# Performance work log

Hardware: AMD Instinct MI355X
Metric: run time of the kernel (lower is better)

Reference implementation:

```python
import jax, jax.numpy as jnp
import numpy as np

HIDDEN = 3584
NUM_HEADS = 28
NUM_KV_HEADS = 4
HEAD_DIM = 128
ROPE_THETA = 1000000.0
B, S = 2, 2048


def setup_inputs() -> dict:
    key = jax.random.key(0)
    k1, k2, k3, k4 = jax.random.split(key, 4)
    q_size = NUM_HEADS * HEAD_DIM
    kv_size = NUM_KV_HEADS * HEAD_DIM
    return {
        "positions": jnp.arange(B * S, dtype=jnp.int32).reshape(B, S),
        "hidden_states": jax.random.normal(k1, (B, S, HIDDEN), dtype=jnp.float32),
        "w_qkv": jax.random.normal(k2, (HIDDEN, q_size + 2 * kv_size), dtype=jnp.float32) * (HIDDEN ** -0.5),
        "b_qkv": jax.random.normal(k3, (q_size + 2 * kv_size,), dtype=jnp.float32) * 0.02,
        "w_o": jax.random.normal(k4, (q_size, HIDDEN), dtype=jnp.float32) * (q_size ** -0.5),
    }


def _rope_cos_sin(positions):
    # NeoX-style rotary embedding, rotary_dim == head_dim
    half = HEAD_DIM // 2
    inv_freq = 1.0 / (ROPE_THETA ** (jnp.arange(0, half, dtype=jnp.float32) * 2.0 / HEAD_DIM))
    angles = positions.astype(jnp.float32)[..., None] * inv_freq  # [B, S, half]
    return jnp.cos(angles), jnp.sin(angles)


def _apply_rope(x, cos, sin):
    # x: [B, S, H, D]; cos/sin: [B, S, half] -> broadcast over heads
    x1, x2 = jnp.split(x, 2, axis=-1)
    c = cos[:, :, None, :]
    s = sin[:, :, None, :]
    return jnp.concatenate([x1 * c - x2 * s, x2 * c + x1 * s], axis=-1)


def reference(positions, hidden_states, w_qkv, b_qkv, w_o):
    q_size = NUM_HEADS * HEAD_DIM
    kv_size = NUM_KV_HEADS * HEAD_DIM
    scaling = HEAD_DIM ** -0.5
    groups = NUM_HEADS // NUM_KV_HEADS

    qkv = hidden_states @ w_qkv + b_qkv  # [B, S, q+2kv]
    q, k, v = jnp.split(qkv, [q_size, q_size + kv_size], axis=-1)
    q = q.reshape(B, S, NUM_HEADS, HEAD_DIM)
    k = k.reshape(B, S, NUM_KV_HEADS, HEAD_DIM)
    v = v.reshape(B, S, NUM_KV_HEADS, HEAD_DIM)

    cos, sin = _rope_cos_sin(positions)
    q = _apply_rope(q, cos, sin)
    k = _apply_rope(k, cos, sin)

    # GQA: group query heads over kv heads. q: [B, S, Hkv, G, D]
    qg = q.reshape(B, S, NUM_KV_HEADS, groups, HEAD_DIM)
    scores = jnp.einsum("bqhgd,bkhd->bhgqk", qg, k) * scaling  # [B, Hkv, G, S, S]
    causal = jnp.tril(jnp.ones((S, S), dtype=bool))
    scores = jnp.where(causal, scores, jnp.finfo(scores.dtype).min)
    probs = jax.nn.softmax(scores, axis=-1)
    o = jnp.einsum("bhgqk,bkhd->bqhgd", probs, v)  # [B, S, Hkv, G, D]
    o = o.reshape(B, S, NUM_HEADS * HEAD_DIM)
    return o @ w_o  # [B, S, HIDDEN]
```

## Files before the change

### kernel.cpp

```cpp
#include <hip/hip_runtime.h>

typedef unsigned short u16;
typedef unsigned int u32;
typedef __bf16 bf16x8 __attribute__((ext_vector_type(8)));
typedef float f32x4 __attribute__((ext_vector_type(4)));

#define NHEAD 28
#define NKVH 4
#define HD 128
#define NB 2
#define NS 2048
#define NTOK 4096
#define HIDDEN_DIM 3584
#define QKVW 4608
#define QSZ 3584
#define KOFF 3584
#define VOFF 4096
#define VSLAB (NTOK * 512)
#define NJOBS 896
#define ATTN_BLOCKS 768
#define QSCALE_L2E 0.12751744f

__device__ __forceinline__ float bf2f(u16 u) {
  u32 x = ((u32)u) << 16; float f; __builtin_memcpy(&f, &x, 4); return f;
}
__device__ __forceinline__ u16 f2bf(float f) {
  u32 x; __builtin_memcpy(&x, &f, 4);
  x += 0x7FFFu + ((x >> 16) & 1u);
  return (u16)(x >> 16);
}
__device__ __forceinline__ u32 pack2bf(float a, float b) {
  __bf16 lo = (__bf16)a, hi = (__bf16)b;
  u16 ul, uh;
  __builtin_memcpy(&ul, &lo, 2); __builtin_memcpy(&uh, &hi, 2);
  return (u32)ul | ((u32)uh << 16);
}
__device__ __forceinline__ void async16(const void* g, void* lds) {
  __builtin_amdgcn_global_load_lds((const __attribute__((address_space(1))) void*)g,
                                   (__attribute__((address_space(3))) void*)lds,
                                   16, 0, 0);
}

#define SB __builtin_amdgcn_sched_barrier(0)
#define BAR do { SB; __builtin_amdgcn_s_barrier(); SB; } while (0)

__global__ void cast_f32_bf16(const float* __restrict__ in, u16* __restrict__ out) {
  int i = (blockIdx.x * 256 + threadIdx.x) * 4;
  float4 v = *(const float4*)(in + i);
  u32 p0 = (u32)f2bf(v.x) | ((u32)f2bf(v.y) << 16);
  u32 p1 = (u32)f2bf(v.z) | ((u32)f2bf(v.w) << 16);
  uint2 r; r.x = p0; r.y = p1;
  *(uint2*)(out + i) = r;
}

__global__ void transpose_cast(const float* __restrict__ in, u16* __restrict__ out,
                               int R, int C) {
  __shared__ float tile[32][33];
  int tx = threadIdx.x & 31, ty = threadIdx.x >> 5;
  int c0 = blockIdx.x * 32, r0 = blockIdx.y * 32;
#pragma unroll
  for (int i = 0; i < 32; i += 8)
    tile[ty + i][tx] = in[(size_t)(r0 + ty + i) * C + c0 + tx];
  __syncthreads();
#pragma unroll
  for (int i = 0; i < 32; i += 8)
    out[(size_t)(c0 + ty + i) * R + r0 + tx] = f2bf(tile[tx][ty + i]);
}

__global__ void rope_table(const int* __restrict__ positions,
                           float* __restrict__ cs, float* __restrict__ sn,
                           int* __restrict__ ctr) {
  if (blockIdx.x == 0 && threadIdx.x == 0) *ctr = 0;
  int idx = blockIdx.x * 256 + threadIdx.x;
  int t = idx >> 6, i = idx & 63;
  float p = (float)positions[t];
  float inv = expf(-(float)i * (13.815510557964274f / 64.f));
  float a = p * inv;
  cs[idx] = cosf(a);
  sn[idx] = sinf(a);
}

__global__ void rope_kernel(u16* __restrict__ qkv, const float* __restrict__ cs,
                            const float* __restrict__ sn) {
  const int gtid = blockIdx.x * 256 + threadIdx.x;
  const int hr = gtid >> 4;
  const int sub = gtid & 15;
  const int t = hr >> 5, hh = hr & 31;
  const size_t base = (size_t)t * QKVW +
                      (hh < NHEAD ? hh * HD : KOFF + (hh - NHEAD) * HD);
  const int d0 = sub * 4;
  uint2 xa = *(const uint2*)(qkv + base + d0);
  uint2 xb = *(const uint2*)(qkv + base + 64 + d0);
  float4 c = *(const float4*)(cs + t * 64 + d0);
  float4 s = *(const float4*)(sn + t * 64 + d0);
  float x1[4], x2[4];
  x1[0] = bf2f((u16)xa.x); x1[1] = bf2f((u16)(xa.x >> 16));
  x1[2] = bf2f((u16)xa.y); x1[3] = bf2f((u16)(xa.y >> 16));
  x2[0] = bf2f((u16)xb.x); x2[1] = bf2f((u16)(xb.x >> 16));
  x2[2] = bf2f((u16)xb.y); x2[3] = bf2f((u16)(xb.y >> 16));
  const float cc[4] = {c.x, c.y, c.z, c.w};
  const float ss[4] = {s.x, s.y, s.z, s.w};
  const float sc = (hh < NHEAD) ? QSCALE_L2E : 1.0f;
  float y1[4], y2[4];
#pragma unroll
  for (int i = 0; i < 4; ++i) {
    y1[i] = (x1[i] * cc[i] - x2[i] * ss[i]) * sc;
    y2[i] = (x2[i] * cc[i] + x1[i] * ss[i]) * sc;
  }
  uint2 ra, rb;
  ra.x = pack2bf(y1[0], y1[1]); ra.y = pack2bf(y1[2], y1[3]);
  rb.x = pack2bf(y2[0], y2[1]); rb.y = pack2bf(y2[2], y2[3]);
  *(uint2*)(qkv + base + d0) = ra;
  *(uint2*)(qkv + base + 64 + d0) = rb;
}

template <int MODE>
__global__ __launch_bounds__(512, 2) void gemm256(
    const u16* __restrict__ A, const u16* __restrict__ Bt,
    const float* __restrict__ bias, u16* __restrict__ outb,
    float* __restrict__ outf, int M, int Next, int Kst, int ldc, int NT) {
  __shared__ __align__(16) u16 Al[2][256 * 64];
  __shared__ __align__(16) u16 Bl[2][256 * 64];
  const int tid = threadIdx.x;
  const int l = tid & 63, w = tid >> 6;
  const int g = l >> 4, r = l & 15;
  const int wm = w >> 2, wn = w & 3;
  const int nbx = Next >> 8;
  const int cpx = (int)gridDim.x >> 3;
  const int bid = ((int)blockIdx.x & 7) * cpx + ((int)blockIdx.x >> 3);
  int bx, by, kbase;
  float* outp = outf;
  if (MODE == 2) {
    const int tps = nbx * (M >> 8);
    const int ks = bid / tps, rem = bid % tps;
    by = rem / nbx; bx = rem % nbx;
    kbase = ks * (NT << 6);
    outp = outf + (size_t)ks * M * Next;
  } else {
    bx = bid % nbx; by = bid / nbx; kbase = 0;
  }
  const int row0 = by * 256, col0 = bx * 256;

  f32x4 acc[8][4] = {};
  bf16x8 af[4][2];
  bf16x8 bfr[2][2][2];

  auto stageU = [&](const u16* mb, int base0, char* ldsMat, int h, int t) {
#pragma unroll
    for (int q = 0; q < 2; ++q) {
      const int idx = q * 512 + tid;
      const int rho = h * 128 + (idx >> 3);
      const int sl = (idx & 7) ^ (rho & 7);
      async16(mb + (size_t)(base0 + rho) * Kst + kbase + t * 64 + sl * 8,
              ldsMat + (size_t)(t & 1) * 32768 + h * 16384 + idx * 16);
    }
  };

#define READ_A(s, rh)                                                           \
  _Pragma("unroll") for (int fr = 0; fr < 4; ++fr) {                            \
    const int row_ = (rh) * 128 + wm * 64 + fr * 16 + r;                        \
    _Pragma("unroll") for (int kk = 0; kk < 2; ++kk) {                          \
      const int sl_ = (kk * 4 + g) ^ (row_ & 7);                                \
      af[fr][kk] = *(const bf16x8*)((const char*)Al + (s) * 32768 +             \
                                    row_ * 128 + sl_ * 16);                     \
    }                                                                           \
  }
#define READ_B(s, ch)                                                           \
  _Pragma("unroll") for (int fc = 0; fc < 2; ++fc) {                            \
    const int col_ = (ch) * 128 + wn * 32 + fc * 16 + r;                        \
    _Pragma("unroll") for (int kk = 0; kk < 2; ++kk) {                          \
      const int sl_ = (kk * 4 + g) ^ (col_ & 7);                                \
      bfr[ch][fc][kk] = *(const bf16x8*)((const char*)Bl + (s) * 32768 +        \
                                         col_ * 128 + sl_ * 16);                \
    }                                                                           \
  }
#define MFMA_Q(rh, ch)                                                          \
  __builtin_amdgcn_s_setprio(1);                                                \
  _Pragma("unroll") for (int fr = 0; fr < 4; ++fr)                              \
  _Pragma("unroll") for (int fc = 0; fc < 2; ++fc)                              \
  _Pragma("unroll") for (int kk = 0; kk < 2; ++kk)                              \
    acc[(rh) * 4 + fr][(ch) * 2 + fc] = __builtin_amdgcn_mfma_f32_16x16x32_bf16( \
        af[fr][kk], bfr[ch][fc][kk], acc[(rh) * 4 + fr][(ch) * 2 + fc], 0, 0, 0);\
  __builtin_amdgcn_s_setprio(0);

  stageU(A, row0, (char*)Al, 0, 0); stageU(A, row0, (char*)Al, 1, 0);
  stageU(Bt, col0, (char*)Bl, 0, 0); stageU(Bt, col0, (char*)Bl, 1, 0);
  stageU(A, row0, (char*)Al, 0, 1); stageU(Bt, col0, (char*)Bl, 0, 1);
  SB; asm volatile("s_waitcnt vmcnt(4)" ::: "memory");
  BAR;

  for (int t = 0; t < NT; ++t) {
    const int s = t & 1;
    READ_A(s, 0); READ_B(s, 0);
    if (t + 1 < NT) stageU(A, row0, (char*)Al, 1, t + 1);
    BAR; MFMA_Q(0, 0); BAR;
    READ_B(s, 1);
    if (t + 1 < NT) stageU(Bt, col0, (char*)Bl, 1, t + 1);
    BAR; MFMA_Q(0, 1); BAR;
    READ_A(s, 1);
    if (t + 2 < NT) stageU(A, row0, (char*)Al, 0, t + 2);
    BAR; MFMA_Q(1, 0); BAR;
    if (t + 2 < NT) stageU(Bt, col0, (char*)Bl, 0, t + 2);
    BAR; MFMA_Q(1, 1);
    if (t < NT - 2)        { SB; asm volatile("s_waitcnt vmcnt(4)" ::: "memory"); }
    else if (t == NT - 2)  { SB; asm volatile("s_waitcnt vmcnt(0)" ::: "memory"); }
    BAR;
  }
  SB; asm volatile("s_waitcnt vmcnt(0)" ::: "memory");

#pragma unroll
  for (int m = 0; m < 8; ++m) {
    const int row = row0 + (m >> 2) * 128 + wm * 64 + (m & 3) * 16 + g * 4;
#pragma unroll
    for (int n = 0; n < 4; ++n) {
      const int col = col0 + (n >> 1) * 128 + wn * 32 + (n & 1) * 16 + r;
      const float bb = (MODE == 0) ? bias[col] : 0.f;
#pragma unroll
      for (int j = 0; j < 4; ++j) {
        float v = acc[m][n][j] + bb;
        if (MODE == 0) outb[(size_t)(row + j) * ldc + col] = f2bf(v);
        else           outp[(size_t)(row + j) * ldc + col] = v;
      }
    }
  }
}

__global__ void v_reduce(const float* __restrict__ slabs, const float* __restrict__ bias,
                         u16* __restrict__ vtg) {
  __shared__ float tile[32][33];
  const int tx = threadIdx.x & 31, ty = threadIdx.x >> 5;
  const int c0 = blockIdx.x * 32;
  const int r0 = blockIdx.y * 32;
#pragma unroll
  for (int i = 0; i < 32; i += 8) {
    const size_t idx = (size_t)(r0 + ty + i) * 512 + c0 + tx;
    float s = slabs[idx] + slabs[idx + VSLAB] + slabs[idx + 2 * VSLAB] +
              slabs[idx + 3 * VSLAB];
    tile[ty + i][tx] = s + bias[VOFF + c0 + tx];
  }
  __syncthreads();
#pragma unroll
  for (int i = 0; i < 32; i += 8) {
    const int col = c0 + ty + i;
    const int row = r0 + tx;
    vtg[((size_t)((((row >> 11) * NKVH) + (col >> 7)) * HD + (col & 127))) * NS +
        (row & 2047)] = f2bf(tile[tx][ty + i]);
  }
}

__global__ __launch_bounds__(512) void attn_kernel(const u16* __restrict__ qkv,
                                                   const u16* __restrict__ vtg,
                                                   u16* __restrict__ Oh,
                                                   int* __restrict__ ctr) {
  __shared__ __align__(16) u16 Ks[2][64 * 128];
  __shared__ __align__(16) u16 Vt[128 * 64];
  __shared__ int s_job;
  const int tid = threadIdx.x, l = tid & 63, w = tid >> 6;
  const int g = l >> 4, r = l & 15;
  const int srcA = r + ((l & 16) << 1);
  const int srcB = srcA + 16;
  const bool hi = (l & 32) != 0;

  for (;;) {
    if (tid == 0) s_job = atomicAdd(ctr, 1);
    __syncthreads();
    const int jid = s_job;
    if (jid >= NJOBS) return;
    const int qtr = jid / 56;
    const int qt = 15 - qtr;
    const int bh = jid - qtr * 56;
    const int h = bh % NHEAD, b = bh / NHEAD;
    const int kvh = h / 7;
    const int q0 = qt * 128;

    const int qrow = q0 + w * 16 + r;
    const size_t qbase = (size_t)(b * NS + qrow) * QKVW + h * HD;
    bf16x8 qf[4];
#pragma unroll
    for (int ks = 0; ks < 4; ++ks)
      qf[ks] = *(const bf16x8*)(qkv + qbase + ks * 32 + g * 8);

    const u16* kb0 = qkv + (size_t)(b * NS) * QKVW + KOFF + kvh * HD;
    const u16* vb0 = vtg + (size_t)((b * NKVH + kvh) * HD) * NS;

    f32x4 oacc[8] = {};
    float mrun = -1e30f, lsum = 0.f;

    const int nkv = 2 * qt + 2;

    auto stageK = [&](u16* kdst, int kv0) {
#pragma unroll
      for (int i = 0; i < 2; ++i) {
        const int li = (w * 2 + i) * 64 + l;
        const int rr = li >> 4, c = li & 15;
        async16(kb0 + (size_t)(kv0 + rr) * QKVW + ((c ^ (rr & 7)) << 3),
                (char*)kdst + (w * 2 + i) * 1024);
      }
    };
    auto stageV = [&](int kv0) {
#pragma unroll
      for (int i = 0; i < 2; ++i) {
        const int li = (w * 2 + i) * 64 + l;
        const int d = li >> 3, c = li & 7;
        async16(vb0 + (size_t)d * NS + kv0 + ((c ^ (d & 7)) << 3),
                (char*)Vt + (w * 2 + i) * 1024);
      }
    };

    stageK(Ks[0], 0);
    int cur = 0;

    for (int kvt = 0; kvt < nkv; ++kvt) {
      const int kv0 = kvt * 64;
      asm volatile("s_waitcnt vmcnt(0) lgkmcnt(0)" ::: "memory");
      __builtin_amdgcn_s_barrier();
      __builtin_amdgcn_sched_barrier(0);

      stageV(kv0);
      const bool haveNext = (kvt + 1 < nkv);
      if (haveNext) stageK(Ks[cur ^ 1], kv0 + 64);

      const bool active = kv0 <= q0 + w * 16 + 15;

      union { u32 wrd[4]; bf16x8 v; } pf[2];
      if (active) {
        f32x4 sacc[4] = {};
        const char* ksB = (const char*)Ks[cur];
        __builtin_amdgcn_s_setprio(1);
#pragma unroll
        for (int n = 0; n < 4; ++n) {
          const int key = n * 16 + r;
          const int sw = (key & 7) << 4;
#pragma unroll
          for (int ks = 0; ks < 4; ++ks) {
            bf16x8 kf = *(const bf16x8*)(ksB + key * 256 + ((ks * 64 + g * 16) ^ sw));
            sacc[n] = __builtin_amdgcn_mfma_f32_16x16x32_bf16(kf, qf[ks], sacc[n], 0, 0, 0);
          }
        }
        __builtin_amdgcn_s_setprio(0);
        if (kv0 + 63 > q0 + w * 16) {
#pragma unroll
          for (int n = 0; n < 4; ++n) {
            const int key_g = kv0 + n * 16 + g * 4;
#pragma unroll
            for (int j = 0; j < 4; ++j)
              if (key_g + j > qrow) sacc[n][j] = -1e30f;
          }
        }
        float mx = fmaxf(fmaxf(sacc[0][0], sacc[0][1]), fmaxf(sacc[0][2], sacc[0][3]));
#pragma unroll
        for (int n = 1; n < 4; ++n)
          mx = fmaxf(mx, fmaxf(fmaxf(sacc[n][0], sacc[n][1]), fmaxf(sacc[n][2], sacc[n][3])));
        if (!__all(mx <= mrun + 8.0f)) {
          mx = fmaxf(mx, __shfl_xor(mx, 16, 64));
          mx = fmaxf(mx, __shfl_xor(mx, 32, 64));
          const float mnew = fmaxf(mrun, mx);
          const float scale = __builtin_amdgcn_exp2f(mrun - mnew);
          mrun = mnew;
          lsum *= scale;
#pragma unroll
          for (int dt = 0; dt < 8; ++dt) oacc[dt] *= scale;
        }
#pragma unroll
        for (int n = 0; n < 4; ++n)
#pragma unroll
          for (int j = 0; j < 4; ++j) {
            float p = __builtin_amdgcn_exp2f(sacc[n][j] - mrun);
            sacc[n][j] = p;
            lsum += p;
          }

        u32 pk[4][2];
#pragma unroll
        for (int n = 0; n < 4; ++n) {
          pk[n][0] = pack2bf(sacc[n][0], sacc[n][1]);
          pk[n][1] = pack2bf(sacc[n][2], sacc[n][3]);
        }
#pragma unroll
        for (int ks2 = 0; ks2 < 2; ++ks2) {
          const int n0 = 2 * ks2, n1 = 2 * ks2 + 1;
#pragma unroll
          for (int hh2 = 0; hh2 < 2; ++hh2) {
            u32 a0 = (u32)__shfl((int)pk[n0][hh2], srcA, 64);
            u32 a1 = (u32)__shfl((int)pk[n1][hh2], srcA, 64);
            pf[ks2].wrd[hh2] = hi ? a1 : a0;
            u32 b0 = (u32)__shfl((int)pk[n0][hh2], srcB, 64);
            u32 b1 = (u32)__shfl((int)pk[n1][hh2], srcB, 64);
            pf[ks2].wrd[2 + hh2] = hi ? b1 : b0;
          }
        }
      }

      if (haveNext) asm volatile("s_waitcnt vmcnt(2)" ::: "memory");
      else          asm volatile("s_waitcnt vmcnt(0)" ::: "memory");
      __builtin_amdgcn_s_barrier();
      __builtin_amdgcn_sched_barrier(0);
      if (active) {
        const char* vtB = (const char*)Vt;
        __builtin_amdgcn_s_setprio(1);
#pragma unroll
        for (int ks2 = 0; ks2 < 2; ++ks2) {
#pragma unroll
          for (int dt = 0; dt < 8; ++dt) {
            const int d = dt * 16 + r;
            bf16x8 vf = *(const bf16x8*)(vtB + d * 128 +
                                         ((ks2 * 64 + g * 16) ^ ((d & 7) << 4)));
            oacc[dt] = __builtin_amdgcn_mfma_f32_16x16x32_bf16(vf, pf[ks2].v, oacc[dt], 0, 0, 0);
          }
        }
        __builtin_amdgcn_s_setprio(0);
      }
      cur ^= 1;
    }

    float lr = lsum;
    lr += __shfl_xor(lr, 16, 64);
    lr += __shfl_xor(lr, 32, 64);
    const float inv = 1.f / lr;
    const size_t obase = (size_t)(b * NS + qrow) * QSZ + h * HD;
#pragma unroll
    for (int dt = 0; dt < 8; ++dt) {
      uint2 r2;
      r2.x = pack2bf(oacc[dt][0] * inv, oacc[dt][1] * inv);
      r2.y = pack2bf(oacc[dt][2] * inv, oacc[dt][3] * inv);
      *(uint2*)(Oh + obase + dt * 16 + 4 * g) = r2;
    }
  }
}

extern "C" void kernel_launch(void* const* d_in, const int* in_sizes, int n_in,
                              void* d_out, int out_size, void* d_ws, size_t ws_size,
                              hipStream_t stream) {
  const int* positions = (const int*)d_in[0];
  const float* hidden = (const float*)d_in[1];
  const float* w_qkv = (const float*)d_in[2];
  const float* b_qkv = (const float*)d_in[3];
  const float* w_o = (const float*)d_in[4];
  float* out = (float*)d_out;

  char* ws = (char*)d_ws;
  const size_t XB_OFF = 0;
  const size_t WQT_OFF = 29360128;
  const size_t QKV_OFF = WQT_OFF + 33030144;
  const size_t CS_OFF = QKV_OFF + 37748736;
  const size_t SN_OFF = CS_OFF + 1048576;
  const size_t CTR_OFF = SN_OFF + 1048576;
  const size_t WS_NEED = CTR_OFF + 64;
  if (ws_size < WS_NEED) return;

  u16* Xb = (u16*)(ws + XB_OFF);
  u16* WoT = (u16*)(ws + XB_OFF);
  u16* WqT = (u16*)(ws + WQT_OFF);
  u16* Oh = (u16*)(ws + WQT_OFF);
  u16* qkvb = (u16*)(ws + QKV_OFF);
  float* cs = (float*)(ws + CS_OFF);
  float* sn = (float*)(ws + SN_OFF);
  int* ctr = (int*)(ws + CTR_OFF);
  u16* vtg = (u16*)d_out;
  float* vslabs = (float*)((char*)d_out + 4194304);

  cast_f32_bf16<<<14336, 256, 0, stream>>>(hidden, Xb);
  transpose_cast<<<dim3(QKVW / 32, HIDDEN_DIM / 32), 256, 0, stream>>>(w_qkv, WqT, HIDDEN_DIM, QKVW);
  rope_table<<<(NTOK * 64) / 256, 256, 0, stream>>>(positions, cs, sn, ctr);

  gemm256<0><<<256, 512, 0, stream>>>(
      Xb, WqT, b_qkv, qkvb, nullptr, NTOK, 4096, HIDDEN_DIM, QKVW, HIDDEN_DIM / 64);

  gemm256<2><<<128, 512, 0, stream>>>(
      Xb, WqT + (size_t)VOFF * HIDDEN_DIM, nullptr, nullptr, vslabs,
      NTOK, 512, HIDDEN_DIM, 512, HIDDEN_DIM / 64 / 4);

  v_reduce<<<dim3(512 / 32, NTOK / 32), 256, 0, stream>>>(vslabs, b_qkv, vtg);

  rope_kernel<<<(NTOK * 32 * 16) / 256, 256, 0, stream>>>(qkvb, cs, sn);

  transpose_cast<<<dim3(HIDDEN_DIM / 32, QSZ / 32), 256, 0, stream>>>(w_o, WoT, QSZ, HIDDEN_DIM);

  attn_kernel<<<ATTN_BLOCKS, 512, 0, stream>>>(qkvb, vtg, Oh, ctr);

  gemm256<1><<<(HIDDEN_DIM / 256) * (NTOK / 256), 512, 0, stream>>>(
      Oh, WoT, nullptr, nullptr, out, NTOK, HIDDEN_DIM, QSZ, HIDDEN_DIM, QSZ / 64);
}
```

Before: 442.0 us.

## Double-buffer V tiles and prefetch next K/V together, dropping mid-iteration barrier

V staging moves to a double-buffered LDS array, so the next tile's K and V are both prefetched at the top of each iteration. This removes the second barrier and wait between the QK and PV phases. Global load addresses are precomputed once per job and advanced by pointer increments. Attention grid size drops from 768 to 512 blocks, since the extra LDS per block lowers occupancy.

```diff
diff --git a/kernel.cpp b/kernel.cpp
--- a/kernel.cpp
+++ b/kernel.cpp
@@ -18,7 +18,7 @@
 #define VOFF 4096
 #define VSLAB (NTOK * 512)
 #define NJOBS 896
-#define ATTN_BLOCKS 768
+#define ATTN_BLOCKS 512
 #define QSCALE_L2E 0.12751744f
 
 __device__ __forceinline__ float bf2f(u16 u) {
@@ -253,7 +253,7 @@
                                                    u16* __restrict__ Oh,
                                                    int* __restrict__ ctr) {
   __shared__ __align__(16) u16 Ks[2][64 * 128];
-  __shared__ __align__(16) u16 Vt[128 * 64];
+  __shared__ __align__(16) u16 Vt[2][128 * 64];
   __shared__ int s_job;
   const int tid = threadIdx.x, l = tid & 63, w = tid >> 6;
   const int g = l >> 4, r = l & 15;
@@ -283,46 +283,51 @@
     const u16* kb0 = qkv + (size_t)(b * NS) * QKVW + KOFF + kvh * HD;
     const u16* vb0 = vtg + (size_t)((b * NKVH + kvh) * HD) * NS;
 
+    const u16* kap[2];
+    const u16* vap[2];
+#pragma unroll
+    for (int i = 0; i < 2; ++i) {
+      const int li = (w * 2 + i) * 64 + l;
+      const int rr = li >> 4, c = li & 15;
+      kap[i] = kb0 + (size_t)rr * QKVW + ((c ^ (rr & 7)) << 3);
+      const int d = li >> 3, c2 = li & 7;
+      vap[i] = vb0 + (size_t)d * NS + ((c2 ^ (d & 7)) << 3);
+    }
+
     f32x4 oacc[8] = {};
     float mrun = -1e30f, lsum = 0.f;
 
     const int nkv = 2 * qt + 2;
 
-    auto stageK = [&](u16* kdst, int kv0) {
+    auto stageK = [&](u16* kdst) {
 #pragma unroll
       for (int i = 0; i < 2; ++i) {
-        const int li = (w * 2 + i) * 64 + l;
-        const int rr = li >> 4, c = li & 15;
-        async16(kb0 + (size_t)(kv0 + rr) * QKVW + ((c ^ (rr & 7)) << 3),
-                (char*)kdst + (w * 2 + i) * 1024);
+        async16(kap[i], (char*)kdst + (w * 2 + i) * 1024);
+        kap[i] += 64 * QKVW;
       }
     };
-    auto stageV = [&](int kv0) {
+    auto stageV = [&](u16* vdst) {
 #pragma unroll
       for (int i = 0; i < 2; ++i) {
-        const int li = (w * 2 + i) * 64 + l;
-        const int d = li >> 3, c = li & 7;
-        async16(vb0 + (size_t)d * NS + kv0 + ((c ^ (d & 7)) << 3),
-                (char*)Vt + (w * 2 + i) * 1024);
+        async16(vap[i], (char*)vdst + (w * 2 + i) * 1024);
+        vap[i] += 64;
       }
     };
 
-    stageK(Ks[0], 0);
+    stageK(Ks[0]); stageV(Vt[0]);
     int cur = 0;
 
     for (int kvt = 0; kvt < nkv; ++kvt) {
       const int kv0 = kvt * 64;
-      asm volatile("s_waitcnt vmcnt(0) lgkmcnt(0)" ::: "memory");
+      asm volatile("s_waitcnt vmcnt(0)" ::: "memory");
       __builtin_amdgcn_s_barrier();
       __builtin_amdgcn_sched_barrier(0);
 
-      stageV(kv0);
       const bool haveNext = (kvt + 1 < nkv);
-      if (haveNext) stageK(Ks[cur ^ 1], kv0 + 64);
+      if (haveNext) { stageK(Ks[cur ^ 1]); stageV(Vt[cur ^ 1]); }
 
       const bool active = kv0 <= q0 + w * 16 + 15;
 
-      union { u32 wrd[4]; bf16x8 v; } pf[2];
       if (active) {
         f32x4 sacc[4] = {};
         const char* ksB = (const char*)Ks[cur];
@@ -376,6 +381,7 @@
           pk[n][0] = pack2bf(sacc[n][0], sacc[n][1]);
           pk[n][1] = pack2bf(sacc[n][2], sacc[n][3]);
         }
+        union { u32 wrd[4]; bf16x8 v; } pf[2];
 #pragma unroll
         for (int ks2 = 0; ks2 < 2; ++ks2) {
           const int n0 = 2 * ks2, n1 = 2 * ks2 + 1;
@@ -389,14 +395,8 @@
             pf[ks2].wrd[2 + hh2] = hi ? b1 : b0;
           }
         }
-      }
-
-      if (haveNext) asm volatile("s_waitcnt vmcnt(2)" ::: "memory");
-      else          asm volatile("s_waitcnt vmcnt(0)" ::: "memory");
-      __builtin_amdgcn_s_barrier();
-      __builtin_amdgcn_sched_barrier(0);
-      if (active) {
-        const char* vtB = (const char*)Vt;
+
+        const char* vtB = (const char*)Vt[cur];
         __builtin_amdgcn_s_setprio(1);
 #pragma unroll
         for (int ks2 = 0; ks2 < 2; ++ks2) {
```

New measurement: 434.0 us. No clear change (-1.8%).

## Switch attention to 32x32x16 MFMA with 4 waves of 32 query rows

Applied to the files above, without the earlier changes.

The attention kernel moves from 8 waves each handling 16 query rows with 16x16x32 MFMAs to 4 waves each handling 32 rows with 32x32x16 MFMAs. The P fragment relayout drops the multiple shuffles per step in favour of v_permlane32_swap. Staging addresses are precomputed once and advanced by a pointer increment. The aim is fewer LDS reads per FLOP and less shuffle and index overhead, at the cost of higher register pressure and fewer waves per block for hiding latency.

```diff
diff --git a/kernel.cpp b/kernel.cpp
--- a/kernel.cpp
+++ b/kernel.cpp
@@ -4,6 +4,7 @@
 typedef unsigned int u32;
 typedef __bf16 bf16x8 __attribute__((ext_vector_type(8)));
 typedef float f32x4 __attribute__((ext_vector_type(4)));
+typedef float f32x16 __attribute__((ext_vector_type(16)));
 
 #define NHEAD 28
 #define NKVH 4
@@ -248,7 +249,7 @@
   }
 }
 
-__global__ __launch_bounds__(512) void attn_kernel(const u16* __restrict__ qkv,
+__global__ __launch_bounds__(256) void attn_kernel(const u16* __restrict__ qkv,
                                                    const u16* __restrict__ vtg,
                                                    u16* __restrict__ Oh,
                                                    int* __restrict__ ctr) {
@@ -256,10 +257,7 @@
   __shared__ __align__(16) u16 Vt[128 * 64];
   __shared__ int s_job;
   const int tid = threadIdx.x, l = tid & 63, w = tid >> 6;
-  const int g = l >> 4, r = l & 15;
-  const int srcA = r + ((l & 16) << 1);
-  const int srcB = srcA + 16;
-  const bool hi = (l & 32) != 0;
+  const int hi = l >> 5, lo5 = l & 31, l7 = l & 7;
 
   for (;;) {
     if (tid == 0) s_job = atomicAdd(ctr, 1);
@@ -273,41 +271,48 @@
     const int kvh = h / 7;
     const int q0 = qt * 128;
 
-    const int qrow = q0 + w * 16 + r;
+    const int qrow = q0 + w * 32 + lo5;
     const size_t qbase = (size_t)(b * NS + qrow) * QKVW + h * HD;
-    bf16x8 qf[4];
-#pragma unroll
-    for (int ks = 0; ks < 4; ++ks)
-      qf[ks] = *(const bf16x8*)(qkv + qbase + ks * 32 + g * 8);
+    bf16x8 qf[8];
+#pragma unroll
+    for (int ks = 0; ks < 8; ++ks)
+      qf[ks] = *(const bf16x8*)(qkv + qbase + ks * 16 + hi * 8);
 
     const u16* kb0 = qkv + (size_t)(b * NS) * QKVW + KOFF + kvh * HD;
     const u16* vb0 = vtg + (size_t)((b * NKVH + kvh) * HD) * NS;
 
-    f32x4 oacc[8] = {};
+    const u16* kap[4];
+    const u16* vap[4];
+#pragma unroll
+    for (int i = 0; i < 4; ++i) {
+      const int li = (w * 4 + i) * 64 + l;
+      const int rr = li >> 4, c = li & 15;
+      kap[i] = kb0 + (size_t)rr * QKVW + ((c ^ (rr & 7)) << 3);
+      const int d = li >> 3, c2 = li & 7;
+      vap[i] = vb0 + (size_t)d * NS + ((c2 ^ (d & 7)) << 3);
+    }
+
+    f32x16 oacc[4] = {};
     float mrun = -1e30f, lsum = 0.f;
 
     const int nkv = 2 * qt + 2;
 
-    auto stageK = [&](u16* kdst, int kv0) {
-#pragma unroll
-      for (int i = 0; i < 2; ++i) {
-        const int li = (w * 2 + i) * 64 + l;
-        const int rr = li >> 4, c = li & 15;
-        async16(kb0 + (size_t)(kv0 + rr) * QKVW + ((c ^ (rr & 7)) << 3),
-                (char*)kdst + (w * 2 + i) * 1024);
+    auto stageK = [&](u16* kdst) {
+#pragma unroll
+      for (int i = 0; i < 4; ++i) {
+        async16(kap[i], (char*)kdst + (w * 4 + i) * 1024);
+        kap[i] += 64 * QKVW;
       }
     };
-    auto stageV = [&](int kv0) {
-#pragma unroll
-      for (int i = 0; i < 2; ++i) {
-        const int li = (w * 2 + i) * 64 + l;
-        const int d = li >> 3, c = li & 7;
-        async16(vb0 + (size_t)d * NS + kv0 + ((c ^ (d & 7)) << 3),
-                (char*)Vt + (w * 2 + i) * 1024);
+    auto stageV = [&]() {
+#pragma unroll
+      for (int i = 0; i < 4; ++i) {
+        async16(vap[i], (char*)Vt + (w * 4 + i) * 1024);
+        vap[i] += 64;
       }
     };
 
-    stageK(Ks[0], 0);
+    stageK(Ks[0]);
     int cur = 0;
 
     for (int kvt = 0; kvt < nkv; ++kvt) {
@@ -316,82 +321,67 @@
       __builtin_amdgcn_s_barrier();
       __builtin_amdgcn_sched_barrier(0);
 
-      stageV(kv0);
+      stageV();
       const bool haveNext = (kvt + 1 < nkv);
-      if (haveNext) stageK(Ks[cur ^ 1], kv0 + 64);
-
-      const bool active = kv0 <= q0 + w * 16 + 15;
-
-      union { u32 wrd[4]; bf16x8 v; } pf[2];
+      if (haveNext) stageK(Ks[cur ^ 1]);
+
+      const bool active = kv0 <= q0 + w * 32 + 31;
+
+      u32 pk[2][8];
       if (active) {
-        f32x4 sacc[4] = {};
+        f32x16 sacc[2] = {};
         const char* ksB = (const char*)Ks[cur];
         __builtin_amdgcn_s_setprio(1);
 #pragma unroll
-        for (int n = 0; n < 4; ++n) {
-          const int key = n * 16 + r;
-          const int sw = (key & 7) << 4;
-#pragma unroll
-          for (int ks = 0; ks < 4; ++ks) {
-            bf16x8 kf = *(const bf16x8*)(ksB + key * 256 + ((ks * 64 + g * 16) ^ sw));
-            sacc[n] = __builtin_amdgcn_mfma_f32_16x16x32_bf16(kf, qf[ks], sacc[n], 0, 0, 0);
+        for (int kblk = 0; kblk < 2; ++kblk) {
+          const int row = kblk * 32 + lo5;
+#pragma unroll
+          for (int ks = 0; ks < 8; ++ks) {
+            const int slot = (ks * 2 + hi) ^ l7;
+            bf16x8 kf = *(const bf16x8*)(ksB + row * 256 + slot * 16);
+            sacc[kblk] = __builtin_amdgcn_mfma_f32_32x32x16_bf16(kf, qf[ks], sacc[kblk], 0, 0, 0);
           }
         }
         __builtin_amdgcn_s_setprio(0);
-        if (kv0 + 63 > q0 + w * 16) {
-#pragma unroll
-          for (int n = 0; n < 4; ++n) {
-            const int key_g = kv0 + n * 16 + g * 4;
-#pragma unroll
-            for (int j = 0; j < 4; ++j)
-              if (key_g + j > qrow) sacc[n][j] = -1e30f;
-          }
+        if (kv0 + 63 > q0 + w * 32) {
+#pragma unroll
+          for (int kblk = 0; kblk < 2; ++kblk)
+#pragma unroll
+            for (int rg = 0; rg < 16; ++rg) {
+              const int key_g = kv0 + kblk * 32 + (rg & 3) + 8 * (rg >> 2) + 4 * hi;
+              if (key_g > qrow) sacc[kblk][rg] = -1e30f;
+            }
         }
-        float mx = fmaxf(fmaxf(sacc[0][0], sacc[0][1]), fmaxf(sacc[0][2], sacc[0][3]));
-#pragma unroll
-        for (int n = 1; n < 4; ++n)
-          mx = fmaxf(mx, fmaxf(fmaxf(sacc[n][0], sacc[n][1]), fmaxf(sacc[n][2], sacc[n][3])));
+        float mx = sacc[0][0];
+#pragma unroll
+        for (int kblk = 0; kblk < 2; ++kblk)
+#pragma unroll
+          for (int rg = 0; rg < 16; ++rg) mx = fmaxf(mx, sacc[kblk][rg]);
         if (!__all(mx <= mrun + 8.0f)) {
-          mx = fmaxf(mx, __shfl_xor(mx, 16, 64));
           mx = fmaxf(mx, __shfl_xor(mx, 32, 64));
           const float mnew = fmaxf(mrun, mx);
           const float scale = __builtin_amdgcn_exp2f(mrun - mnew);
           mrun = mnew;
           lsum *= scale;
 #pragma unroll
-          for (int dt = 0; dt < 8; ++dt) oacc[dt] *= scale;
+          for (int d4 = 0; d4 < 4; ++d4) oacc[d4] *= scale;
         }
 #pragma unroll
-        for (int n = 0; n < 4; ++n)
-#pragma unroll
-          for (int j = 0; j < 4; ++j) {
-            float p = __builtin_amdgcn_exp2f(sacc[n][j] - mrun);
-            sacc[n][j] = p;
+        for (int kblk = 0; kblk < 2; ++kblk)
+#pragma unroll
+          for (int rg = 0; rg < 16; ++rg) {
+            float p = __builtin_amdgcn_exp2f(sacc[kblk][rg] - mrun);
+            sacc[kblk][rg] = p;
             lsum += p;
           }
-
-        u32 pk[4][2];
-#pragma unroll
-        for (int n = 0; n < 4; ++n) {
-          pk[n][0] = pack2bf(sacc[n][0], sacc[n][1]);
-          pk[n][1] = pack2bf(sacc[n][2], sacc[n][3]);
-        }
-#pragma unroll
-        for (int ks2 = 0; ks2 < 2; ++ks2) {
-          const int n0 = 2 * ks2, n1 = 2 * ks2 + 1;
-#pragma unroll
-          for (int hh2 = 0; hh2 < 2; ++hh2) {
-            u32 a0 = (u32)__shfl((int)pk[n0][hh2], srcA, 64);
-            u32 a1 = (u32)__shfl((int)pk[n1][hh2], srcA, 64);
-            pf[ks2].wrd[hh2] = hi ? a1 : a0;
-            u32 b0 = (u32)__shfl((int)pk[n0][hh2], srcB, 64);
-            u32 b1 = (u32)__shfl((int)pk[n1][hh2], srcB, 64);
-            pf[ks2].wrd[2 + hh2] = hi ? b1 : b0;
-          }
-        }
-      }
-
-      if (haveNext) asm volatile("s_waitcnt vmcnt(2)" ::: "memory");
+#pragma unroll
+        for (int kblk = 0; kblk < 2; ++kblk)
+#pragma unroll
+          for (int i = 0; i < 8; ++i)
+            pk[kblk][i] = pack2bf(sacc[kblk][2 * i], sacc[kblk][2 * i + 1]);
+      }
+
+      if (haveNext) asm volatile("s_waitcnt vmcnt(4)" ::: "memory");
       else          asm volatile("s_waitcnt vmcnt(0)" ::: "memory");
       __builtin_amdgcn_s_barrier();
       __builtin_amdgcn_sched_barrier(0);
@@ -399,13 +389,23 @@
         const char* vtB = (const char*)Vt;
         __builtin_amdgcn_s_setprio(1);
 #pragma unroll
-        for (int ks2 = 0; ks2 < 2; ++ks2) {
-#pragma unroll
-          for (int dt = 0; dt < 8; ++dt) {
-            const int d = dt * 16 + r;
-            bf16x8 vf = *(const bf16x8*)(vtB + d * 128 +
-                                         ((ks2 * 64 + g * 16) ^ ((d & 7) << 4)));
-            oacc[dt] = __builtin_amdgcn_mfma_f32_16x16x32_bf16(vf, pf[ks2].v, oacc[dt], 0, 0, 0);
+        for (int kblk = 0; kblk < 2; ++kblk) {
+#pragma unroll
+          for (int sub = 0; sub < 2; ++sub) {
+            const int kp = kblk * 2 + sub;
+            u32 a0 = pk[kblk][sub * 4 + 0], a1 = pk[kblk][sub * 4 + 1];
+            u32 a2 = pk[kblk][sub * 4 + 2], a3 = pk[kblk][sub * 4 + 3];
+            asm volatile("v_permlane32_swap_b32 %0, %1" : "+v"(a0), "+v"(a2));
+            asm volatile("v_permlane32_swap_b32 %0, %1" : "+v"(a1), "+v"(a3));
+            union { u32 u[4]; bf16x8 v; } pf;
+            pf.u[0] = a0; pf.u[1] = a1; pf.u[2] = a2; pf.u[3] = a3;
+#pragma unroll
+            for (int dblk = 0; dblk < 4; ++dblk) {
+              const int rowd = dblk * 32 + lo5;
+              const int slot = (kp * 2 + hi) ^ l7;
+              bf16x8 vf = *(const bf16x8*)(vtB + rowd * 128 + slot * 16);
+              oacc[dblk] = __builtin_amdgcn_mfma_f32_32x32x16_bf16(vf, pf.v, oacc[dblk], 0, 0, 0);
+            }
           }
         }
         __builtin_amdgcn_s_setprio(0);
@@ -413,18 +413,19 @@
       cur ^= 1;
     }
 
-    float lr = lsum;
-    lr += __shfl_xor(lr, 16, 64);
-    lr += __shfl_xor(lr, 32, 64);
+    float lr = lsum + __shfl_xor(lsum, 32, 64);
     const float inv = 1.f / lr;
     const size_t obase = (size_t)(b * NS + qrow) * QSZ + h * HD;
 #pragma unroll
-    for (int dt = 0; dt < 8; ++dt) {
-      uint2 r2;
-      r2.x = pack2bf(oacc[dt][0] * inv, oacc[dt][1] * inv);
-      r2.y = pack2bf(oacc[dt][2] * inv, oacc[dt][3] * inv);
-      *(uint2*)(Oh + obase + dt * 16 + 4 * g) = r2;
-    }
+    for (int dblk = 0; dblk < 4; ++dblk)
+#pragma unroll
+      for (int grp = 0; grp < 4; ++grp) {
+        const int d = dblk * 32 + grp * 8 + 4 * hi;
+        uint2 r2;
+        r2.x = pack2bf(oacc[dblk][grp * 4 + 0] * inv, oacc[dblk][grp * 4 + 1] * inv);
+        r2.y = pack2bf(oacc[dblk][grp * 4 + 2] * inv, oacc[dblk][grp * 4 + 3] * inv);
+        *(uint2*)(Oh + obase + d) = r2;
+      }
   }
 }
 
@@ -476,7 +477,7 @@
 
   transpose_cast<<<dim3(HIDDEN_DIM / 32, QSZ / 32), 256, 0, stream>>>(w_o, WoT, QSZ, HIDDEN_DIM);
 
-  attn_kernel<<<ATTN_BLOCKS, 512, 0, stream>>>(qkvb, vtg, Oh, ctr);
+  attn_kernel<<<ATTN_BLOCKS, 256, 0, stream>>>(qkvb, vtg, Oh, ctr);
 
   gemm256<1><<<(HIDDEN_DIM / 256) * (NTOK / 256), 512, 0, stream>>>(
       Oh, WoT, nullptr, nullptr, out, NTOK, HIDDEN_DIM, QSZ, HIDDEN_DIM, QSZ / 64);
```

Result: no change. 443.0 us (+0.2%).
